# Performance work log

Measured on AMD Instinct MI355X. Metric: run time of the kernel, lower is better.

## Reference

```python
import jax, jax.numpy as jnp
import numpy as np

B, C, H, W = 16, 3, 1024, 1024
DENSITY = 0.015
SIGMA = 1.5
K = 5  # blur kernel size
N_FLAKES = int(H * W * DENSITY)  # 15728


def setup_inputs() -> dict:
    key = jax.random.key(0)
    kx, ky, kxs, kr = jax.random.split(key, 4)
    x = jax.random.uniform(kx, (B, C, H, W), dtype=jnp.float32)
    ys = jax.random.randint(ky, (B, N_FLAKES), 0, H, dtype=jnp.int32)
    xs = jax.random.randint(kxs, (B, N_FLAKES), 0, W, dtype=jnp.int32)
    rs = jax.random.randint(kr, (B, N_FLAKES), 1, 4, dtype=jnp.int32)  # radius in {1,2,3}
    return {"x": x, "ys": ys, "xs": xs, "rs": rs}


def reference(x, ys, xs, rs):
    Bb, Cc, Hh, Ww = x.shape
    # --- vectorized flake stamping (replaces per-flake Python loop) ---
    # Each flake writes a (2r+1)x(2r+1) square of 0.95, clipped to image bounds.
    # Max radius is 3 -> enumerate the 7x7 = 49 candidate offsets per flake.
    off = jnp.arange(-3, 4)
    dyg, dxg = jnp.meshgrid(off, off, indexing="ij")
    dy = dyg.reshape(-1)  # [49]
    dx = dxg.reshape(-1)  # [49]
    r = rs[..., None]  # [B, N, 1]
    valid = (jnp.abs(dy) <= r) & (jnp.abs(dx) <= r)  # [B, N, 49]
    # Clamping out-of-bounds coords to the border is equivalent to torch's
    # slice-clipping because the written value is a constant (0.95) and the
    # border pixel is already covered by an in-range offset. Invalid offsets
    # (|d| > r) are redirected to the flake center, which is always stamped.
    yy = jnp.where(valid, jnp.clip(ys[..., None] + dy, 0, Hh - 1), ys[..., None])
    xx = jnp.where(valid, jnp.clip(xs[..., None] + dx, 0, Ww - 1), xs[..., None])
    b = jnp.arange(Bb)[:, None, None]  # [B,1,1]
    out = x.at[b, :, yy, xx].set(0.95)  # stamp all channels

    # --- depthwise 5x5 gaussian blur ---
    coords = jnp.arange(K, dtype=jnp.float32) - K // 2
    g = jnp.exp(-(coords ** 2) / (2.0 * SIGMA ** 2))
    g = g / g.sum()
    kern = jnp.outer(g, g).astype(x.dtype)[None, None]  # [1,1,5,5]
    kern = jnp.broadcast_to(kern, (Cc, 1, K, K))  # depthwise: O=C, I=1
    pad = K // 2
    out = jax.lax.conv_general_dilated(
        out, kern, window_strides=(1, 1), padding=[(pad, pad), (pad, pad)],
        feature_group_count=Cc, dimension_numbers=("NCHW", "OIHW", "NCHW"))
    return jnp.clip(out, 0.0, 1.0)
```

## Files before the change

### kernel.cpp

```cpp
#include <hip/hip_runtime.h>


#define H_ 1024
#define W_ 1024
#define B_ 16
#define C_ 3
#define NF_ 15728
#define MASK_WORDS_PER_B (H_ * W_ / 32)

#define G0 0.12007838f
#define G1 0.23388076f
#define G2 0.29208172f

__global__ void clear_mask_kernel(uint4* __restrict__ mask, int n4) {
    int i = blockIdx.x * blockDim.x + threadIdx.x;
    if (i < n4) mask[i] = make_uint4(0u, 0u, 0u, 0u);
}

__global__ void stamp_kernel(const int* __restrict__ ys, const int* __restrict__ xs,
                             const int* __restrict__ rs, unsigned int* __restrict__ mask) {
    int t = blockIdx.x * blockDim.x + threadIdx.x;
    if (t >= B_ * NF_) return;
    int b = t / NF_;
    int y0 = ys[t], x0 = xs[t], r = rs[t];
    unsigned int* mb = mask + b * MASK_WORDS_PER_B;
    int xlo = max(x0 - r, 0), xhi = min(x0 + r, W_ - 1);
    int ylo = max(y0 - r, 0), yhi = min(y0 + r, H_ - 1);
    for (int y = ylo; y <= yhi; ++y) {
        int i0 = (y << 10) + xlo;
        int i1 = (y << 10) + xhi;
        int w0 = i0 >> 5, w1 = i1 >> 5;
        unsigned int m0 = ~0u << (i0 & 31);
        unsigned int m1 = ~0u >> (31 - (i1 & 31));
        if (w0 == w1) {
            atomicOr(mb + w0, m0 & m1);
        } else {
            atomicOr(mb + w0, m0);
            atomicOr(mb + w1, m1);
        }
    }
}

constexpr int BAND = 32;
constexpr int NITER = BAND + 4;

__global__ __launch_bounds__(256, 4) void blur_kernel(const float* __restrict__ x,
                                                      const unsigned int* __restrict__ mask,
                                                      float* __restrict__ out) {
    const int plane = blockIdx.z;
    const int b = plane / C_;
    const float* xp = x + (size_t)plane * (H_ * W_);
    float* op = out + (size_t)plane * (H_ * W_);
    const unsigned int* mb = mask + b * MASK_WORDS_PER_B;

    const int tid = threadIdx.x;
    const int wv = tid >> 6;
    const int ln = tid & 63;
    const int gx4 = (wv << 8) + (ln << 2);
    const int y0 = blockIdx.y * BAND;

    const bool isL = (ln == 0), isR = (ln == 63);
    const int hoff = isL ? gx4 - 2 : gx4 + 4;
    const bool haloOn = (isL || isR) && ((unsigned)hoff < (unsigned)W_);
    const int mwi = gx4 >> 5, mbit = gx4 & 31;
    const int hwi = hoff >> 5, hbit = hoff & 31;

    float4 acc[5];
    float2 hacc[5];
    #pragma unroll
    for (int s = 0; s < 5; ++s) {
        acc[s] = make_float4(0.f, 0.f, 0.f, 0.f);
        hacc[s] = make_float2(0.f, 0.f);
    }

    float4 px[2];  unsigned int pm[2];
    float2 ph[2];  unsigned int phm[2];
    px[0] = px[1] = make_float4(0.f, 0.f, 0.f, 0.f);
    ph[0] = ph[1] = make_float2(0.f, 0.f);
    pm[0] = pm[1] = 0u; phm[0] = phm[1] = 0u;

    auto load_row = [&](int i, float4& vx, unsigned int& vm,
                        float2& vh, unsigned int& vhm) {
        int gy = y0 - 2 + i;
        if ((unsigned)gy < (unsigned)H_) {
            vx = *(const float4*)(xp + (gy << 10) + gx4);
            vm = mb[(gy << 5) + mwi];
            if (haloOn) {
                vh = *(const float2*)(xp + (gy << 10) + hoff);
                vhm = mb[(gy << 5) + hwi];
            } else { vh = make_float2(0.f, 0.f); vhm = 0u; }
        } else {
            vx = make_float4(0.f, 0.f, 0.f, 0.f); vm = 0u;
            vh = make_float2(0.f, 0.f); vhm = 0u;
        }
    };

    load_row(0, px[0], pm[0], ph[0], phm[0]);
    load_row(1, px[1], pm[1], ph[1], phm[1]);

    #pragma unroll
    for (int i = 0; i < NITER; ++i) {
        float4 vr = px[i & 1];
        unsigned int m = pm[i & 1];
        if ((m >> (mbit + 0)) & 1u) vr.x = 0.95f;
        if ((m >> (mbit + 1)) & 1u) vr.y = 0.95f;
        if ((m >> (mbit + 2)) & 1u) vr.z = 0.95f;
        if ((m >> (mbit + 3)) & 1u) vr.w = 0.95f;
        float2 hr = ph[i & 1];
        unsigned int hm = phm[i & 1];
        if ((hm >> (hbit + 0)) & 1u) hr.x = 0.95f;
        if ((hm >> (hbit + 1)) & 1u) hr.y = 0.95f;

        if (i + 2 < NITER) load_row(i + 2, px[i & 1], pm[i & 1], ph[i & 1], phm[i & 1]);

        #pragma unroll
        for (int d = -2; d <= 2; ++d) {
            int ti = i - 2 + d;
            if (ti < 0 || ti >= BAND) continue;
            const float wk = (d == -2 || d == 2) ? G0 : ((d == -1 || d == 1) ? G1 : G2);
            const int sl = ti % 5;
            acc[sl].x += wk * vr.x; acc[sl].y += wk * vr.y;
            acc[sl].z += wk * vr.z; acc[sl].w += wk * vr.w;
            hacc[sl].x += wk * hr.x; hacc[sl].y += wk * hr.y;
        }

        if (i >= 4) {
            const int ti = i - 4;
            const int sl = ti % 5;
            float4 vb = acc[sl];
            float2 hvb = hacc[sl];
            float az = __shfl_up(vb.z, 1u);
            float aw = __shfl_up(vb.w, 1u);
            float cx = __shfl_down(vb.x, 1u);
            float cy = __shfl_down(vb.y, 1u);
            az = isL ? hvb.x : az;  aw = isL ? hvb.y : aw;
            cx = isR ? hvb.x : cx;  cy = isR ? hvb.y : cy;
            float4 o;
            o.x = G0 * (az + vb.z) + G1 * (aw + vb.y) + G2 * vb.x;
            o.y = G0 * (aw + vb.w) + G1 * (vb.x + vb.z) + G2 * vb.y;
            o.z = G0 * (vb.x + cx) + G1 * (vb.y + vb.w) + G2 * vb.z;
            o.w = G0 * (vb.y + cy) + G1 * (vb.z + cx) + G2 * vb.w;
            o.x = fminf(fmaxf(o.x, 0.0f), 1.0f);
            o.y = fminf(fmaxf(o.y, 0.0f), 1.0f);
            o.z = fminf(fmaxf(o.z, 0.0f), 1.0f);
            o.w = fminf(fmaxf(o.w, 0.0f), 1.0f);
            *(float4*)(op + ((y0 + ti) << 10) + gx4) = o;
            acc[sl] = make_float4(0.f, 0.f, 0.f, 0.f);
            hacc[sl] = make_float2(0.f, 0.f);
        }
    }
}

extern "C" void kernel_launch(void* const* d_in, const int* in_sizes, int n_in,
                              void* d_out, int out_size, void* d_ws, size_t ws_size,
                              hipStream_t stream) {
    const float* x  = (const float*)d_in[0];
    const int*   ys = (const int*)d_in[1];
    const int*   xs = (const int*)d_in[2];
    const int*   rs = (const int*)d_in[3];
    float* out = (float*)d_out;
    unsigned int* mask = (unsigned int*)d_ws;

    int n4 = B_ * MASK_WORDS_PER_B / 4;
    clear_mask_kernel<<<dim3((n4 + 255) / 256), dim3(256), 0, stream>>>((uint4*)mask, n4);

    int nst = B_ * NF_;
    stamp_kernel<<<dim3((nst + 255) / 256), dim3(256), 0, stream>>>(ys, xs, rs, mask);

    dim3 grid(1, H_ / BAND, B_ * C_);
    blur_kernel<<<grid, dim3(256), 0, stream>>>(x, mask, out);
}
```

Measured before the change: 423.3 us.

## Load all band rows upfront with smaller bands and nontemporal output stores

Shrinks the row band per block from 32 to 8, so the grid has four times as many blocks. Instead of a two-row rolling prefetch with scattered accumulators, each thread now issues all 12 input row loads (plus halo and mask words) at the start and then computes a direct 5-tap vertical sum per output row. Output stores become nontemporal so they do not displace cached input. The aim is more memory-level parallelism and occupancy, traded against more halo re-reads per output row (12 rows loaded for 8 written instead of 36 for 32) and more registers held per thread.

```diff
diff --git a/kernel.cpp b/kernel.cpp
--- a/kernel.cpp
+++ b/kernel.cpp
@@ -11,6 +11,8 @@
 #define G0 0.12007838f
 #define G1 0.23388076f
 #define G2 0.29208172f
+
+typedef float nat_f4 __attribute__((ext_vector_type(4)));
 
 __global__ void clear_mask_kernel(uint4* __restrict__ mask, int n4) {
     int i = blockIdx.x * blockDim.x + threadIdx.x;
@@ -41,8 +43,8 @@
     }
 }
 
-constexpr int BAND = 32;
-constexpr int NITER = BAND + 4;
+constexpr int BAND = 8;
+constexpr int ROWS = BAND + 4;
 
 __global__ __launch_bounds__(256, 4) void blur_kernel(const float* __restrict__ x,
                                                       const unsigned int* __restrict__ mask,
@@ -65,89 +67,69 @@
     const int mwi = gx4 >> 5, mbit = gx4 & 31;
     const int hwi = hoff >> 5, hbit = hoff & 31;
 
-    float4 acc[5];
-    float2 hacc[5];
+    float4 raw[ROWS];
+    float2 hraw[ROWS];
+    unsigned int rm[ROWS], hrm[ROWS];
+
     #pragma unroll
-    for (int s = 0; s < 5; ++s) {
-        acc[s] = make_float4(0.f, 0.f, 0.f, 0.f);
-        hacc[s] = make_float2(0.f, 0.f);
+    for (int r = 0; r < ROWS; ++r) {
+        int gy = y0 - 2 + r;
+        if ((unsigned)gy < (unsigned)H_) {
+            raw[r] = *(const float4*)(xp + (gy << 10) + gx4);
+            rm[r]  = mb[(gy << 5) + mwi];
+            if (haloOn) {
+                hraw[r] = *(const float2*)(xp + (gy << 10) + hoff);
+                hrm[r]  = mb[(gy << 5) + hwi];
+            } else { hraw[r] = make_float2(0.f, 0.f); hrm[r] = 0u; }
+        } else {
+            raw[r] = make_float4(0.f, 0.f, 0.f, 0.f); rm[r] = 0u;
+            hraw[r] = make_float2(0.f, 0.f); hrm[r] = 0u;
+        }
     }
 
-    float4 px[2];  unsigned int pm[2];
-    float2 ph[2];  unsigned int phm[2];
-    px[0] = px[1] = make_float4(0.f, 0.f, 0.f, 0.f);
-    ph[0] = ph[1] = make_float2(0.f, 0.f);
-    pm[0] = pm[1] = 0u; phm[0] = phm[1] = 0u;
-
-    auto load_row = [&](int i, float4& vx, unsigned int& vm,
-                        float2& vh, unsigned int& vhm) {
-        int gy = y0 - 2 + i;
-        if ((unsigned)gy < (unsigned)H_) {
-            vx = *(const float4*)(xp + (gy << 10) + gx4);
-            vm = mb[(gy << 5) + mwi];
-            if (haloOn) {
-                vh = *(const float2*)(xp + (gy << 10) + hoff);
-                vhm = mb[(gy << 5) + hwi];
-            } else { vh = make_float2(0.f, 0.f); vhm = 0u; }
-        } else {
-            vx = make_float4(0.f, 0.f, 0.f, 0.f); vm = 0u;
-            vh = make_float2(0.f, 0.f); vhm = 0u;
-        }
-    };
-
-    load_row(0, px[0], pm[0], ph[0], phm[0]);
-    load_row(1, px[1], pm[1], ph[1], phm[1]);
+    #pragma unroll
+    for (int r = 0; r < ROWS; ++r) {
+        unsigned int m = rm[r];
+        if ((m >> (mbit + 0)) & 1u) raw[r].x = 0.95f;
+        if ((m >> (mbit + 1)) & 1u) raw[r].y = 0.95f;
+        if ((m >> (mbit + 2)) & 1u) raw[r].z = 0.95f;
+        if ((m >> (mbit + 3)) & 1u) raw[r].w = 0.95f;
+        unsigned int hm = hrm[r];
+        if ((hm >> (hbit + 0)) & 1u) hraw[r].x = 0.95f;
+        if ((hm >> (hbit + 1)) & 1u) hraw[r].y = 0.95f;
+    }
 
     #pragma unroll
-    for (int i = 0; i < NITER; ++i) {
-        float4 vr = px[i & 1];
-        unsigned int m = pm[i & 1];
-        if ((m >> (mbit + 0)) & 1u) vr.x = 0.95f;
-        if ((m >> (mbit + 1)) & 1u) vr.y = 0.95f;
-        if ((m >> (mbit + 2)) & 1u) vr.z = 0.95f;
-        if ((m >> (mbit + 3)) & 1u) vr.w = 0.95f;
-        float2 hr = ph[i & 1];
-        unsigned int hm = phm[i & 1];
-        if ((hm >> (hbit + 0)) & 1u) hr.x = 0.95f;
-        if ((hm >> (hbit + 1)) & 1u) hr.y = 0.95f;
+    for (int t = 0; t < BAND; ++t) {
+        float4 vb;
+        vb.x = G0 * (raw[t].x + raw[t + 4].x) + G1 * (raw[t + 1].x + raw[t + 3].x) + G2 * raw[t + 2].x;
+        vb.y = G0 * (raw[t].y + raw[t + 4].y) + G1 * (raw[t + 1].y + raw[t + 3].y) + G2 * raw[t + 2].y;
+        vb.z = G0 * (raw[t].z + raw[t + 4].z) + G1 * (raw[t + 1].z + raw[t + 3].z) + G2 * raw[t + 2].z;
+        vb.w = G0 * (raw[t].w + raw[t + 4].w) + G1 * (raw[t + 1].w + raw[t + 3].w) + G2 * raw[t + 2].w;
+        float2 hvb;
+        hvb.x = G0 * (hraw[t].x + hraw[t + 4].x) + G1 * (hraw[t + 1].x + hraw[t + 3].x) + G2 * hraw[t + 2].x;
+        hvb.y = G0 * (hraw[t].y + hraw[t + 4].y) + G1 * (hraw[t + 1].y + hraw[t + 3].y) + G2 * hraw[t + 2].y;
 
-        if (i + 2 < NITER) load_row(i + 2, px[i & 1], pm[i & 1], ph[i & 1], phm[i & 1]);
+        float az = __shfl_up(vb.z, 1u);
+        float aw = __shfl_up(vb.w, 1u);
+        float cx = __shfl_down(vb.x, 1u);
+        float cy = __shfl_down(vb.y, 1u);
+        az = isL ? hvb.x : az;  aw = isL ? hvb.y : aw;
+        cx = isR ? hvb.x : cx;  cy = isR ? hvb.y : cy;
 
-        #pragma unroll
-        for (int d = -2; d <= 2; ++d) {
-            int ti = i - 2 + d;
-            if (ti < 0 || ti >= BAND) continue;
-            const float wk = (d == -2 || d == 2) ? G0 : ((d == -1 || d == 1) ? G1 : G2);
-            const int sl = ti % 5;
-            acc[sl].x += wk * vr.x; acc[sl].y += wk * vr.y;
-            acc[sl].z += wk * vr.z; acc[sl].w += wk * vr.w;
-            hacc[sl].x += wk * hr.x; hacc[sl].y += wk * hr.y;
-        }
+        float4 o;
+        o.x = G0 * (az + vb.z) + G1 * (aw + vb.y) + G2 * vb.x;
+        o.y = G0 * (aw + vb.w) + G1 * (vb.x + vb.z) + G2 * vb.y;
+        o.z = G0 * (vb.x + cx) + G1 * (vb.y + vb.w) + G2 * vb.z;
+        o.w = G0 * (vb.y + cy) + G1 * (vb.z + cx) + G2 * vb.w;
+        o.x = fminf(fmaxf(o.x, 0.0f), 1.0f);
+        o.y = fminf(fmaxf(o.y, 0.0f), 1.0f);
+        o.z = fminf(fmaxf(o.z, 0.0f), 1.0f);
+        o.w = fminf(fmaxf(o.w, 0.0f), 1.0f);
 
-        if (i >= 4) {
-            const int ti = i - 4;
-            const int sl = ti % 5;
-            float4 vb = acc[sl];
-            float2 hvb = hacc[sl];
-            float az = __shfl_up(vb.z, 1u);
-            float aw = __shfl_up(vb.w, 1u);
-            float cx = __shfl_down(vb.x, 1u);
-            float cy = __shfl_down(vb.y, 1u);
-            az = isL ? hvb.x : az;  aw = isL ? hvb.y : aw;
-            cx = isR ? hvb.x : cx;  cy = isR ? hvb.y : cy;
-            float4 o;
-            o.x = G0 * (az + vb.z) + G1 * (aw + vb.y) + G2 * vb.x;
-            o.y = G0 * (aw + vb.w) + G1 * (vb.x + vb.z) + G2 * vb.y;
-            o.z = G0 * (vb.x + cx) + G1 * (vb.y + vb.w) + G2 * vb.z;
-            o.w = G0 * (vb.y + cy) + G1 * (vb.z + cx) + G2 * vb.w;
-            o.x = fminf(fmaxf(o.x, 0.0f), 1.0f);
-            o.y = fminf(fmaxf(o.y, 0.0f), 1.0f);
-            o.z = fminf(fmaxf(o.z, 0.0f), 1.0f);
-            o.w = fminf(fmaxf(o.w, 0.0f), 1.0f);
-            *(float4*)(op + ((y0 + ti) << 10) + gx4) = o;
-            acc[sl] = make_float4(0.f, 0.f, 0.f, 0.f);
-            hacc[sl] = make_float2(0.f, 0.f);
-        }
+        nat_f4 ov;
+        ov.x = o.x; ov.y = o.y; ov.z = o.z; ov.w = o.w;
+        __builtin_nontemporal_store(ov, (nat_f4*)(op + ((y0 + t) << 10) + gx4));
     }
 }
 
```

After: 406.6 us. 1.04x faster.
